# Optimization experiments

Measured on AMD Instinct MI355X. Metric: run time of the kernel, lower is better.

The kernel has to match this reference:

```python
import jax, jax.numpy as jnp
import numpy as np

D_MODEL = 32; D_STATE = 16; D_CONV = 4; D_INNER = 64; DT_RANK = 2
BATCH = 64; C_IN = 64; PATCH = 32; FEATURE_DIM = 128


def setup_inputs() -> dict:
    key = jax.random.key(0)
    ks = jax.random.split(key, 14)
    def w(k, shape, fan_in):
        return jax.random.normal(k, shape, jnp.float32) * np.float32(1.0 / np.sqrt(fan_in))
    dt_init = jnp.exp(jax.random.uniform(ks[12], (D_INNER,), jnp.float32,
                                         np.float32(np.log(1e-3)), np.float32(np.log(1e-1))))
    return {
        "x": jax.random.normal(ks[0], (BATCH, C_IN, PATCH, PATCH), jnp.float32),
        "conv_w": w(ks[1], (D_MODEL, C_IN), C_IN),
        "conv_b": jnp.zeros((D_MODEL,), jnp.float32),
        "bn_gamma": jnp.ones((D_MODEL,), jnp.float32),
        "bn_beta": jnp.zeros((D_MODEL,), jnp.float32),
        "bn_mean": jnp.zeros((D_MODEL,), jnp.float32),
        "bn_var": jnp.ones((D_MODEL,), jnp.float32),
        "in_proj_w": w(ks[2], (2 * D_INNER, D_MODEL), D_MODEL),
        "conv1d_w": w(ks[3], (D_INNER, D_CONV), D_CONV),
        "conv1d_b": jnp.zeros((D_INNER,), jnp.float32),
        "x_proj_w": w(ks[4], (DT_RANK + 2 * D_STATE, D_INNER), D_INNER),
        "dt_proj_w": w(ks[5], (D_INNER, DT_RANK), DT_RANK),
        "dt_proj_b": jnp.log(jnp.expm1(dt_init)),
        "A_log": jnp.log(jnp.tile(jnp.arange(1, D_STATE + 1, dtype=jnp.float32), (D_INNER, 1))),
        "D_param": jnp.ones((D_INNER,), jnp.float32),
        "out_proj_w": w(ks[6], (D_MODEL, D_INNER), D_INNER),
        "fc_w": w(ks[7], (FEATURE_DIM, D_MODEL), D_MODEL),
        "fc_b": jnp.zeros((FEATURE_DIM,), jnp.float32),
    }


def reference(x, conv_w, conv_b, bn_gamma, bn_beta, bn_mean, bn_var, in_proj_w,
              conv1d_w, conv1d_b, x_proj_w, dt_proj_w, dt_proj_b, A_log, D_param,
              out_proj_w, fc_w, fc_b):
    Bsz = x.shape[0]
    # --- stem: 1x1 conv + BatchNorm (eval stats) + exact GELU ---
    h = jnp.einsum('bchw,dc->bdhw', x, conv_w) + conv_b[:, None, None]
    scale = bn_gamma / jnp.sqrt(bn_var + 1e-5)
    h = (h - bn_mean[:, None, None]) * scale[:, None, None] + bn_beta[:, None, None]
    h = jax.nn.gelu(h, approximate=False)
    u = h.reshape(Bsz, D_MODEL, -1).transpose(0, 2, 1)   # [B, L, d_model], L = H*W
    # --- Mamba block ---
    xz = u @ in_proj_w.T                                  # [B, L, 2*d_inner]
    xm, z = xz[..., :D_INNER], xz[..., D_INNER:]
    # depthwise causal conv1d over the sequence
    xt = jnp.pad(xm.transpose(0, 2, 1), ((0, 0), (0, 0), (D_CONV - 1, 0)))
    xt = jax.lax.conv_general_dilated(xt, conv1d_w[:, None, :], (1,), 'VALID',
                                      feature_group_count=D_INNER,
                                      dimension_numbers=('NCH', 'OIH', 'NCH'))
    xm = jax.nn.silu(xt + conv1d_b[None, :, None]).transpose(0, 2, 1)  # [B, L, d_inner]
    x_dbl = xm @ x_proj_w.T                               # [B, L, dt_rank + 2*d_state]
    dt = jax.nn.softplus(x_dbl[..., :DT_RANK] @ dt_proj_w.T + dt_proj_b)  # [B, L, d_inner]
    Bt = x_dbl[..., DT_RANK:DT_RANK + D_STATE]            # [B, L, d_state]
    Ct = x_dbl[..., DT_RANK + D_STATE:]                   # [B, L, d_state]
    A = -jnp.exp(A_log)                                   # [d_inner, d_state]

    def step(hst, inp):
        u_t, dt_t, B_t, C_t = inp                         # [B,d],[B,d],[B,n],[B,n]
        hst = jnp.exp(dt_t[:, :, None] * A) * hst + (dt_t * u_t)[:, :, None] * B_t[:, None, :]
        return hst, jnp.einsum('bdn,bn->bd', hst, C_t)

    h0 = jnp.zeros((Bsz, D_INNER, D_STATE), xm.dtype)
    _, ys = jax.lax.scan(step, h0, (xm.transpose(1, 0, 2), dt.transpose(1, 0, 2),
                                    Bt.transpose(1, 0, 2), Ct.transpose(1, 0, 2)))
    y = ys.transpose(1, 0, 2) + xm * D_param
    y = y * jax.nn.silu(z)
    out = y @ out_proj_w.T                                # [B, L, d_model]
    pooled = out.mean(axis=1)                             # [B, d_model]
    return pooled @ fc_w.T + fc_b                         # [B, FEATURE_DIM]
```

## Files before the change

kernel.cpp:

```cpp
#include <hip/hip_runtime.h>
#include <hip/hip_bf16.h>
#include <math.h>

#define L 1024
typedef __hip_bfloat16 bf;
typedef __attribute__((ext_vector_type(8))) short short8v;
typedef __attribute__((ext_vector_type(4))) short short4v;

__device__ __forceinline__ float b2f(bf v) { return __bfloat162float(v); }
__device__ __forceinline__ bf f2b(float v) { return __float2bfloat16(v); }
__device__ __forceinline__ float bits2f(short s) {
  union { unsigned u; float f; } cv; cv.u = ((unsigned)(unsigned short)s) << 16; return cv.f;
}
union Pack4 { short4v v; unsigned short e[4]; };
union Pack8 { short8v v; unsigned short e[8]; };
__device__ __forceinline__ unsigned short f2bits(float v) {
  union { bf b; unsigned short u; } cv; cv.b = __float2bfloat16(v); return cv.u;
}

__global__ __launch_bounds__(256, 2) void k_front(
    const float* __restrict__ x, const float* __restrict__ conv_w,
    const float* __restrict__ conv_b, const float* __restrict__ gamma,
    const float* __restrict__ beta, const float* __restrict__ mean,
    const float* __restrict__ var, const float* __restrict__ ipw,
    bf* __restrict__ xm, bf* __restrict__ z) {
  __shared__ float xs[64 * 65];
  __shared__ float hsh[64][34];
  int t = threadIdx.x;
  int b = blockIdx.x >> 4;
  int l0 = (blockIdx.x & 15) << 6;
  const float* xg = x + (size_t)b * 65536 + l0;
#pragma unroll
  for (int k = 0; k < 16; ++k) {
    int i = t + k * 256;
    int c = i >> 6, ll = i & 63;
    xs[c * 65 + ll] = xg[(size_t)c * L + ll];
  }
  __syncthreads();
  int lq = t & 63;
  int q = __builtin_amdgcn_readfirstlane(t >> 6);
  int l = l0 | lq;
  float hacc[8];
#pragma unroll
  for (int dd = 0; dd < 8; ++dd) hacc[dd] = conv_b[q * 8 + dd];
#pragma unroll
  for (int c4 = 0; c4 < 16; ++c4) {
    float x0 = xs[(c4 * 4 + 0) * 65 + lq];
    float x1 = xs[(c4 * 4 + 1) * 65 + lq];
    float x2 = xs[(c4 * 4 + 2) * 65 + lq];
    float x3 = xs[(c4 * 4 + 3) * 65 + lq];
#pragma unroll
    for (int dd = 0; dd < 8; ++dd) {
      const float* w = conv_w + (q * 8 + dd) * 64 + c4 * 4;
      hacc[dd] = fmaf(x0, w[0], fmaf(x1, w[1],
                 fmaf(x2, w[2], fmaf(x3, w[3], hacc[dd]))));
    }
  }
#pragma unroll
  for (int dd = 0; dd < 8; ++dd) {
    int d = q * 8 + dd;
    float sc = gamma[d] * rsqrtf(var[d] + 1e-5f);
    float acc = (hacc[dd] - mean[d]) * sc + beta[d];
    hsh[lq][d] = 0.5f * acc * (1.0f + erff(acc * 0.70710678118654752f));
  }
  __syncthreads();
  float h[32];
#pragma unroll
  for (int d = 0; d < 32; ++d) h[d] = hsh[lq][d];
  if (q < 2) {
    short8v* xr8 = (short8v*)(xm + ((size_t)b * 1024 + l) * 64) + q * 4;
#pragma unroll
    for (int j8 = 0; j8 < 4; ++j8) {
      Pack8 p;
#pragma unroll
      for (int e = 0; e < 8; ++e) {
        int j = q * 32 + j8 * 8 + e;
        float acc = 0.f;
#pragma unroll
        for (int d = 0; d < 32; ++d) acc = fmaf(h[d], ipw[j * 32 + d], acc);
        p.e[e] = f2bits(acc);
      }
      xr8[j8] = p.v;
    }
  } else {
    bf* zp = z + (size_t)b * 65536 + l;
#pragma unroll
    for (int jj = 0; jj < 32; ++jj) {
      int j = (q - 2) * 32 + jj;
      float acc = 0.f;
#pragma unroll
      for (int d = 0; d < 32; ++d) acc = fmaf(h[d], ipw[(j + 64) * 32 + d], acc);
      zp[(size_t)j * L] = f2b(acc);
    }
  }
}

__global__ __launch_bounds__(128) void k_mid(
    const bf* __restrict__ xm, const float* __restrict__ c1w,
    const float* __restrict__ c1b, const float* __restrict__ xpw,
    const float* __restrict__ dtw, const float* __restrict__ dtbp,
    bf* __restrict__ u, bf* __restrict__ dt_o,
    bf* __restrict__ Bt, bf* __restrict__ Ct) {
  int t = threadIdx.x;
  int qk = __builtin_amdgcn_readfirstlane(t >> 6);
  int l = (blockIdx.x & 15) * 64 + (t & 63);
  int b = blockIdx.x >> 4;
  float um[64];
#pragma unroll
  for (int d = 0; d < 64; ++d) um[d] = c1b[d];
#pragma unroll
  for (int k = 0; k < 4; ++k) {
    int lr = l - 3 + k;
    if (lr >= 0) {
      const short8v* row = (const short8v*)(xm + (size_t)b * 65536 + (size_t)lr * 64);
#pragma unroll
      for (int d8 = 0; d8 < 8; ++d8) {
        short8v v = row[d8];
#pragma unroll
        for (int e = 0; e < 8; ++e)
          um[d8 * 8 + e] = fmaf(c1w[(d8 * 8 + e) * 4 + k], bits2f(v[e]), um[d8 * 8 + e]);
      }
    }
  }
#pragma unroll
  for (int d = 0; d < 64; ++d) {
    float s = um[d];
    um[d] = s / (1.f + __expf(-s));
  }
  int i = l & 31, c = l >> 5;
  if (qk == 0) {
    float xd[18];
#pragma unroll
    for (int k = 0; k < 18; ++k) {
      float acc = 0.f;
#pragma unroll
      for (int d = 0; d < 64; ++d) acc = fmaf(um[d], xpw[k * 64 + d], acc);
      xd[k] = acc;
    }
    bf* dp = dt_o + (size_t)b * 65536 + l;
#pragma unroll
    for (int d = 0; d < 64; ++d) {
      float raw = fmaf(xd[0], dtw[d * 2], fmaf(xd[1], dtw[d * 2 + 1], dtbp[d]));
      float sp = fmaxf(raw, 0.f) + log1pf(__expf(-fabsf(raw)));
      dp[(size_t)d * L] = f2b(sp);
    }
    size_t basei = ((size_t)b * 16384 + (size_t)i * 128 + c * 4) >> 2;
    short4v* B4 = (short4v*)Bt;
#pragma unroll
    for (int n4 = 0; n4 < 4; ++n4) {
      Pack4 pb;
#pragma unroll
      for (int nn = 0; nn < 4; ++nn) pb.e[nn] = f2bits(xd[2 + n4 * 4 + nn]);
      B4[basei + (size_t)n4 * 1024] = pb.v;
    }
  } else {
    bf* up = u + (size_t)b * 65536 + l;
#pragma unroll
    for (int d = 0; d < 64; ++d) up[(size_t)d * L] = f2b(um[d]);
    float xd[16];
#pragma unroll
    for (int k = 0; k < 16; ++k) {
      float acc = 0.f;
#pragma unroll
      for (int d = 0; d < 64; ++d) acc = fmaf(um[d], xpw[(18 + k) * 64 + d], acc);
      xd[k] = acc;
    }
    size_t basei = ((size_t)b * 16384 + (size_t)i * 128 + c * 4) >> 2;
    short4v* C4 = (short4v*)Ct;
#pragma unroll
    for (int n4 = 0; n4 < 4; ++n4) {
      Pack4 pc;
#pragma unroll
      for (int nn = 0; nn < 4; ++nn) pc.e[nn] = f2bits(xd[n4 * 4 + nn]);
      C4[basei + (size_t)n4 * 1024] = pc.v;
    }
  }
}

__global__ __launch_bounds__(256, 2) void k_scan(
    const bf* __restrict__ u, const bf* __restrict__ dt,
    const bf* __restrict__ z, const bf* __restrict__ Bt,
    const bf* __restrict__ Ct, const float* __restrict__ A_log,
    const float* __restrict__ Dp, float* __restrict__ pooled64) {
  __shared__ bf Bsh[16384];
  __shared__ bf Csh[16384];
  int phys = blockIdx.x;
  int b = phys & 63;
  int dgrp = phys >> 6;
  int t = threadIdx.x;
  int d_local = t >> 5, c = t & 31;
  int d = dgrp * 8 + d_local;
  int g = b * 64 + d;

  {
    const short8v* Bg8 = (const short8v*)(Bt + (size_t)b * 16384);
    const short8v* Cg8 = (const short8v*)(Ct + (size_t)b * 16384);
    short8v* Bs8 = (short8v*)Bsh;
    short8v* Cs8 = (short8v*)Csh;
#pragma unroll
    for (int q = 0; q < 8; ++q) {
      Bs8[t + q * 256] = Bg8[t + q * 256];
      Cs8[t + q * 256] = Cg8[t + q * 256];
    }
  }
  __syncthreads();

  float An[16];
#pragma unroll
  for (int n = 0; n < 16; ++n) An[n] = -__expf(A_log[d * 16 + n]);
  const short4v* dps = (const short4v*)(dt + (size_t)g * L + c * 32);
  const short4v* ups = (const short4v*)(u  + (size_t)g * L + c * 32);
  const short4v* zps = (const short4v*)(z  + (size_t)g * L + c * 32);
  const short4v* Bs4 = (const short4v*)Bsh;
  const short4v* Cs4 = (const short4v*)Csh;
  float Dd = Dp[d];

  float h[16], pi[16], q[16];
#pragma unroll
  for (int n = 0; n < 16; ++n) { h[n] = 0.f; pi[n] = 1.f; q[n] = 0.f; }
  float base = 0.f;

#pragma unroll 1
  for (int t4 = 0; t4 < 8; ++t4) {
    short4v d4 = dps[t4], u4 = ups[t4], z4 = zps[t4];
#pragma unroll
    for (int i = 0; i < 4; ++i) {
      int step = t4 * 4 + i;
      float dtv = bits2f(d4[i]);
      float uv  = bits2f(u4[i]);
      float zv  = bits2f(z4[i]);
      float sv  = zv / (1.f + __expf(-zv));
      float du  = dtv * uv;
      int slot = step * 32 + c;
      float y0 = 0.f, y1 = 0.f;
#pragma unroll
      for (int n4 = 0; n4 < 4; ++n4) {
        short4v bq = Bs4[n4 * 1024 + slot];
        short4v cq = Cs4[n4 * 1024 + slot];
#pragma unroll
        for (int nn = 0; nn < 4; ++nn) {
          int n = n4 * 4 + nn;
          float a = __expf(dtv * An[n]);
          float Bv = bits2f(bq[nn]);
          float Cv = bits2f(cq[nn]);
          h[n] = fmaf(a, h[n], du * Bv);
          pi[n] *= a;
          if (nn & 1) y1 = fmaf(h[n], Cv, y1); else y0 = fmaf(h[n], Cv, y0);
          q[n] = fmaf(sv * pi[n], Cv, q[n]);
        }
      }
      base = fmaf(sv, (y0 + y1) + uv * Dd, base);
    }
  }

#pragma unroll
  for (int s = 1; s < 32; s <<= 1) {
    bool act = (c >= s);
#pragma unroll
    for (int n = 0; n < 16; ++n) {
      float Po = __shfl_up(pi[n], (unsigned)s, 32);
      float Oo = __shfl_up(h[n], (unsigned)s, 32);
      if (act) { h[n] = fmaf(pi[n], Oo, h[n]); pi[n] *= Po; }
    }
  }
  float pooled = base;
#pragma unroll
  for (int n = 0; n < 16; ++n) {
    float v = __shfl_up(h[n], 1u, 32);
    float hin = (c == 0) ? 0.f : v;
    pooled = fmaf(q[n], hin, pooled);
  }
#pragma unroll
  for (int s = 1; s < 32; s <<= 1) pooled += __shfl_xor(pooled, s, 32);
  if (c == 0) pooled64[g] = pooled;
}

__global__ __launch_bounds__(128) void k_fc(
    const float* __restrict__ pooled64, const float* __restrict__ opw,
    const float* __restrict__ fcw, const float* __restrict__ fcb,
    float* __restrict__ out) {
  __shared__ float p64[64];
  __shared__ float o32[32];
  int b = blockIdx.x, t = threadIdx.x;
  if (t < 64) p64[t] = pooled64[b * 64 + t];
  __syncthreads();
  if (t < 32) {
    float s = 0.f;
#pragma unroll
    for (int d0 = 0; d0 < 64; ++d0) s = fmaf(p64[d0], opw[t * 64 + d0], s);
    o32[t] = s * (1.f / 1024.f);
  }
  __syncthreads();
  float acc = fcb[t];
#pragma unroll
  for (int j = 0; j < 32; ++j) acc = fmaf(o32[j], fcw[t * 32 + j], acc);
  out[b * 128 + t] = acc;
}

extern "C" void kernel_launch(void* const* d_in, const int* in_sizes, int n_in,
                              void* d_out, int out_size, void* d_ws, size_t ws_size,
                              hipStream_t stream) {
  const float* x      = (const float*)d_in[0];
  const float* conv_w = (const float*)d_in[1];
  const float* conv_b = (const float*)d_in[2];
  const float* bn_g   = (const float*)d_in[3];
  const float* bn_b   = (const float*)d_in[4];
  const float* bn_m   = (const float*)d_in[5];
  const float* bn_v   = (const float*)d_in[6];
  const float* ipw    = (const float*)d_in[7];
  const float* c1w    = (const float*)d_in[8];
  const float* c1b    = (const float*)d_in[9];
  const float* xpw    = (const float*)d_in[10];
  const float* dtw    = (const float*)d_in[11];
  const float* dtbp   = (const float*)d_in[12];
  const float* A_log  = (const float*)d_in[13];
  const float* Dp     = (const float*)d_in[14];
  const float* opw    = (const float*)d_in[15];
  const float* fcw    = (const float*)d_in[16];
  const float* fcb    = (const float*)d_in[17];

  char* ws = (char*)d_ws;
  bf* xmb = (bf*)(ws + 0);
  bf* zb  = (bf*)(ws + 8388608);
  bf* ub  = (bf*)(ws + 16777216);
  bf* dtb = (bf*)(ws + 25165824);
  bf* Btb = (bf*)(ws + 33554432);
  bf* Ctb = (bf*)(ws + 35651584);
  float* pooled = (float*)(ws + 37748736);

  hipLaunchKernelGGL(k_front, dim3(1024), dim3(256), 0, stream,
                     x, conv_w, conv_b, bn_g, bn_b, bn_m, bn_v, ipw, xmb, zb);
  hipLaunchKernelGGL(k_mid, dim3(1024), dim3(128), 0, stream,
                     xmb, c1w, c1b, xpw, dtw, dtbp, ub, dtb, Btb, Ctb);
  hipLaunchKernelGGL(k_scan, dim3(512), dim3(256), 0, stream,
                     ub, dtb, zb, Btb, Ctb, A_log, Dp, pooled);
  hipLaunchKernelGGL(k_fc, dim3(64), dim3(128), 0, stream,
                     pooled, opw, fcw, fcb, (float*)d_out);
}
```

Measured before the change: 128.8 us.

## Split k_mid work across four waves with shared-memory exchange of conv outputs

k_mid now runs 256 threads per block. Each wave computes the depthwise conv and SiLU for 16 of the 64 channels, writes u, and shares the results through LDS. After a barrier, the x_proj projections are rebalanced across the four waves: wave 0 does dt and softplus, and the other waves split the B and C rows in 4-row jobs. This reduces per-thread register pressure and serial work, raising parallelism, at the cost of an LDS round-trip and a __syncthreads.

Result: no change. 130.3 us (+1.1%).

```diff
diff --git a/kernel.cpp b/kernel.cpp
--- a/kernel.cpp
+++ b/kernel.cpp
@@ -95,84 +95,88 @@
   }
 }
 
-__global__ __launch_bounds__(128) void k_mid(
+__global__ __launch_bounds__(256, 2) void k_mid(
     const bf* __restrict__ xm, const float* __restrict__ c1w,
     const float* __restrict__ c1b, const float* __restrict__ xpw,
     const float* __restrict__ dtw, const float* __restrict__ dtbp,
     bf* __restrict__ u, bf* __restrict__ dt_o,
     bf* __restrict__ Bt, bf* __restrict__ Ct) {
+  __shared__ float ush[64][65];
   int t = threadIdx.x;
-  int qk = __builtin_amdgcn_readfirstlane(t >> 6);
-  int l = (blockIdx.x & 15) * 64 + (t & 63);
+  int lq = t & 63;
+  int q = __builtin_amdgcn_readfirstlane(t >> 6);
   int b = blockIdx.x >> 4;
-  float um[64];
-#pragma unroll
-  for (int d = 0; d < 64; ++d) um[d] = c1b[d];
+  int l = ((blockIdx.x & 15) << 6) | lq;
+  float um[16];
+#pragma unroll
+  for (int dd = 0; dd < 16; ++dd) um[dd] = c1b[q * 16 + dd];
 #pragma unroll
   for (int k = 0; k < 4; ++k) {
     int lr = l - 3 + k;
     if (lr >= 0) {
-      const short8v* row = (const short8v*)(xm + (size_t)b * 65536 + (size_t)lr * 64);
-#pragma unroll
-      for (int d8 = 0; d8 < 8; ++d8) {
-        short8v v = row[d8];
-#pragma unroll
-        for (int e = 0; e < 8; ++e)
-          um[d8 * 8 + e] = fmaf(c1w[(d8 * 8 + e) * 4 + k], bits2f(v[e]), um[d8 * 8 + e]);
+      const short8v* row = (const short8v*)(xm + ((size_t)b * 1024 + lr) * 64 + q * 16);
+      short8v v0 = row[0], v1 = row[1];
+#pragma unroll
+      for (int e = 0; e < 8; ++e) {
+        um[e]     = fmaf(c1w[(q * 16 + e) * 4 + k],     bits2f(v0[e]), um[e]);
+        um[8 + e] = fmaf(c1w[(q * 16 + 8 + e) * 4 + k], bits2f(v1[e]), um[8 + e]);
       }
     }
   }
-#pragma unroll
-  for (int d = 0; d < 64; ++d) {
-    float s = um[d];
-    um[d] = s / (1.f + __expf(-s));
-  }
+  {
+    bf* up = u + (size_t)b * 65536 + l;
+#pragma unroll
+    for (int dd = 0; dd < 16; ++dd) {
+      float s = um[dd];
+      s = s / (1.f + __expf(-s));
+      ush[lq][q * 16 + dd] = s;
+      up[(size_t)(q * 16 + dd) * L] = f2b(s);
+    }
+  }
+  __syncthreads();
+  float um64[64];
+#pragma unroll
+  for (int d = 0; d < 64; ++d) um64[d] = ush[lq][d];
   int i = l & 31, c = l >> 5;
-  if (qk == 0) {
-    float xd[18];
-#pragma unroll
-    for (int k = 0; k < 18; ++k) {
-      float acc = 0.f;
-#pragma unroll
-      for (int d = 0; d < 64; ++d) acc = fmaf(um[d], xpw[k * 64 + d], acc);
-      xd[k] = acc;
+  size_t basei = ((size_t)b * 16384 + (size_t)i * 128 + c * 4) >> 2;
+  if (q == 0) {
+    float xd0 = 0.f, xd1 = 0.f;
+#pragma unroll
+    for (int d = 0; d < 64; ++d) {
+      xd0 = fmaf(um64[d], xpw[d], xd0);
+      xd1 = fmaf(um64[d], xpw[64 + d], xd1);
     }
     bf* dp = dt_o + (size_t)b * 65536 + l;
 #pragma unroll
     for (int d = 0; d < 64; ++d) {
-      float raw = fmaf(xd[0], dtw[d * 2], fmaf(xd[1], dtw[d * 2 + 1], dtbp[d]));
+      float raw = fmaf(xd0, dtw[d * 2], fmaf(xd1, dtw[d * 2 + 1], dtbp[d]));
       float sp = fmaxf(raw, 0.f) + log1pf(__expf(-fabsf(raw)));
       dp[(size_t)d * L] = f2b(sp);
     }
-    size_t basei = ((size_t)b * 16384 + (size_t)i * 128 + c * 4) >> 2;
+  } else {
     short4v* B4 = (short4v*)Bt;
-#pragma unroll
-    for (int n4 = 0; n4 < 4; ++n4) {
-      Pack4 pb;
-#pragma unroll
-      for (int nn = 0; nn < 4; ++nn) pb.e[nn] = f2bits(xd[2 + n4 * 4 + nn]);
-      B4[basei + (size_t)n4 * 1024] = pb.v;
-    }
-  } else {
-    bf* up = u + (size_t)b * 65536 + l;
-#pragma unroll
-    for (int d = 0; d < 64; ++d) up[(size_t)d * L] = f2b(um[d]);
-    float xd[16];
-#pragma unroll
-    for (int k = 0; k < 16; ++k) {
-      float acc = 0.f;
-#pragma unroll
-      for (int d = 0; d < 64; ++d) acc = fmaf(um[d], xpw[(18 + k) * 64 + d], acc);
-      xd[k] = acc;
-    }
-    size_t basei = ((size_t)b * 16384 + (size_t)i * 128 + c * 4) >> 2;
     short4v* C4 = (short4v*)Ct;
 #pragma unroll
-    for (int n4 = 0; n4 < 4; ++n4) {
-      Pack4 pc;
-#pragma unroll
-      for (int nn = 0; nn < 4; ++nn) pc.e[nn] = f2bits(xd[n4 * 4 + nn]);
-      C4[basei + (size_t)n4 * 1024] = pc.v;
+    for (int job = 0; job < 3; ++job) {
+      int kb, n4; short4v* dst;
+      if (q == 1)      { if (job == 0) { dst = B4; kb = 2;  n4 = 0; }
+                         else if (job == 1) { dst = B4; kb = 6;  n4 = 1; }
+                         else { dst = C4; kb = 18; n4 = 0; } }
+      else if (q == 2) { if (job == 0) { dst = B4; kb = 10; n4 = 2; }
+                         else if (job == 1) { dst = B4; kb = 14; n4 = 3; }
+                         else { dst = C4; kb = 22; n4 = 1; } }
+      else             { if (job == 0) { dst = C4; kb = 26; n4 = 2; }
+                         else if (job == 1) { dst = C4; kb = 30; n4 = 3; }
+                         else break; }
+      Pack4 p;
+#pragma unroll
+      for (int nn = 0; nn < 4; ++nn) {
+        float acc = 0.f;
+#pragma unroll
+        for (int d = 0; d < 64; ++d) acc = fmaf(um64[d], xpw[(kb + nn) * 64 + d], acc);
+        p.e[nn] = f2bits(acc);
+      }
+      dst[basei + (size_t)n4 * 1024] = p.v;
     }
   }
 }
@@ -330,7 +334,7 @@
 
   hipLaunchKernelGGL(k_front, dim3(1024), dim3(256), 0, stream,
                      x, conv_w, conv_b, bn_g, bn_b, bn_m, bn_v, ipw, xmb, zb);
-  hipLaunchKernelGGL(k_mid, dim3(1024), dim3(128), 0, stream,
+  hipLaunchKernelGGL(k_mid, dim3(1024), dim3(256), 0, stream,
                      xmb, c1w, c1b, xpw, dtw, dtbp, ub, dtb, Btb, Ctb);
   hipLaunchKernelGGL(k_scan, dim3(512), dim3(256), 0, stream,
                      ub, dtb, zb, Btb, Ctb, A_log, Dp, pooled);
```
